# Kernel optimization log

Hardware: AMD Instinct MI355X
Metric: run time of the kernel (lower is better)

The kernel has to match this reference:

```python
import jax, jax.numpy as jnp
import numpy as np

N = 100000       # nodes
E = 1600000      # edges
V = 50000        # vocab
H = 256          # embedding dim (hsize)
A = 64           # per-head out dim (asize)
NH = 3           # num_heads
G = 64           # graphs in batch


def setup_inputs() -> dict:
    key = jax.random.key(0)
    ks = jax.random.split(key, 12)
    h0 = jax.random.randint(ks[0], (N,), 0, V)
    src = jax.random.randint(ks[1], (E,), 0, N)
    dst = jax.random.randint(ks[2], (E,), 0, N)
    graph_ids = jnp.sort(jax.random.randint(ks[3], (N,), 0, G))
    s = 0.05
    emb = jax.random.normal(ks[4], (V, H), jnp.float32) * s
    W_fc = jax.random.normal(ks[5], (H, NH * A), jnp.float32) * s   # GATConv fc
    attn_l = jax.random.normal(ks[6], (NH, A), jnp.float32) * s
    attn_r = jax.random.normal(ks[7], (NH, A), jnp.float32) * s
    bias_gat = jax.random.normal(ks[8], (NH, A), jnp.float32) * s
    W1 = jax.random.normal(ks[9], (A, 128), jnp.float32) * s
    b1 = jnp.zeros((128,), jnp.float32)
    W2 = jax.random.normal(ks[10], (128, 16), jnp.float32) * s
    b2 = jnp.zeros((16,), jnp.float32)
    return dict(h0=h0, src=src, dst=dst, graph_ids=graph_ids, emb=emb,
                W_fc=W_fc, attn_l=attn_l, attn_r=attn_r, bias_gat=bias_gat,
                W1=W1, b1=b1, W2=W2, b2=b2)


def reference(h0, src, dst, graph_ids, emb, W_fc, attn_l, attn_r, bias_gat,
              W1, b1, W2, b2):
    # embedding lookup
    h1 = emb[h0]                                            # [N, H]
    # GATConv: linear projection per head
    feat = (h1 @ W_fc).reshape(N, NH, A)                    # [N, NH, A]
    el = jnp.einsum('nha,ha->nh', feat, attn_l)             # [N, NH]
    er = jnp.einsum('nha,ha->nh', feat, attn_r)             # [N, NH]
    e = jax.nn.leaky_relu(el[src] + er[dst], 0.2)           # [E, NH]
    # segment softmax over incoming edges of each dst node
    m = jax.ops.segment_max(e, dst, num_segments=N)         # [N, NH]
    e_exp = jnp.exp(e - m[dst])                             # [E, NH]
    denom = jax.ops.segment_sum(e_exp, dst, num_segments=N) # [N, NH]
    alpha = e_exp / denom[dst]                              # [E, NH]
    # scatter-aggregate messages
    msg = alpha[:, :, None] * feat[src]                     # [E, NH, A]
    rst = jax.ops.segment_sum(msg, dst, num_segments=N)     # [N, NH, A]
    rst = rst + bias_gat[None]                              # GATConv bias
    # relu + mean over heads
    h2 = jnp.mean(jax.nn.relu(rst), axis=1)                 # [N, A]
    # MLP predictor: ReLU then Identity
    h3 = jax.nn.relu(h2 @ W1 + b1) @ W2 + b2                # [N, 16]
    # dgl.mean_nodes: per-graph mean readout
    sums = jax.ops.segment_sum(h3, graph_ids, num_segments=G)            # [G, 16]
    counts = jax.ops.segment_sum(jnp.ones((N,), h3.dtype), graph_ids, num_segments=G)
    return sums / jnp.maximum(counts, 1.0)[:, None]         # [G, 16]
```

## Files before the change

kernel.cpp:

```cpp
#include <hip/hip_runtime.h>
#include <hip/hip_bf16.h>

#define NNODES 100000
#define NEDGES 1600000
#define VOCAB 50000
#define HDIM 256
#define ADIM 64
#define NHEADS 3
#define FDIM 192
#define NGRAPH 64
#define NPART 64

#define CONV_ELEMS (HDIM * FDIM + 128 * 64 + 16 * 128)
#define CONV_BLOCKS ((CONV_ELEMS + 255) / 256)
#define HIST_BLOCKS ((NEDGES + 255) / 256)

typedef __attribute__((ext_vector_type(8))) short bf16x8;
typedef __attribute__((ext_vector_type(4))) float f32x4;

__device__ __forceinline__ float bf2f(unsigned short u) {
  return __uint_as_float((unsigned int)u << 16);
}
__device__ __forceinline__ unsigned short f2bf(float f) {
  unsigned int u = __float_as_uint(f);
  u += 0x7FFFu + ((u >> 16) & 1u);
  return (unsigned short)(u >> 16);
}

__global__ __launch_bounds__(256) void conv_hist_kernel(
    const float* __restrict__ Wfc, const float* __restrict__ W1,
    const float* __restrict__ W2, unsigned short* __restrict__ Wt,
    unsigned short* __restrict__ W1t, unsigned short* __restrict__ W2t,
    const int* __restrict__ dst, int* __restrict__ cnt,
    unsigned short* __restrict__ rank16)
{
  if (blockIdx.x < CONV_BLOCKS) {
    int i = blockIdx.x * 256 + threadIdx.x;
    if (i < HDIM * FDIM) {
      int c = i / HDIM, k = i % HDIM;
      Wt[i] = f2bf(Wfc[(size_t)k * FDIM + c]);
    } else if (i < HDIM * FDIM + 128 * 64) {
      int j = i - HDIM * FDIM;
      int c = j / 64, k = j % 64;
      W1t[j] = f2bf(W1[(size_t)k * 128 + c]);
    } else if (i < CONV_ELEMS) {
      int j = i - HDIM * FDIM - 128 * 64;
      int c = j / 128, k = j % 128;
      W2t[j] = f2bf(W2[(size_t)k * 16 + c]);
    }
  } else {
    int e = (blockIdx.x - CONV_BLOCKS) * 256 + threadIdx.x;
    if (e < NEDGES) rank16[e] = (unsigned short)atomicAdd(&cnt[dst[e]], 1);
  }
}

__global__ __launch_bounds__(256) void scan_sum_kernel(
    const int* __restrict__ cnt, int* __restrict__ bsum, int n)
{
  __shared__ int red[256];
  int t = threadIdx.x;
  int base = blockIdx.x * 1024 + t * 4;
  int s = 0;
#pragma unroll
  for (int j = 0; j < 4; ++j) if (base + j < n) s += cnt[base + j];
  red[t] = s;
  __syncthreads();
  for (int o = 128; o > 0; o >>= 1) {
    if (t < o) red[t] += red[t + o];
    __syncthreads();
  }
  if (t == 0) bsum[blockIdx.x] = red[0];
}

__global__ void scan_bsum_kernel(int* bsum, int nb)
{
  if (threadIdx.x == 0 && blockIdx.x == 0) {
    int acc = 0;
    for (int i = 0; i < nb; ++i) { int v = bsum[i]; bsum[i] = acc; acc += v; }
  }
}

__global__ __launch_bounds__(256) void scan_write_kernel(
    const int* __restrict__ cnt, const int* __restrict__ bsum,
    int* __restrict__ offs, int n, int total)
{
  __shared__ int sd[256];
  int t = threadIdx.x;
  int base = blockIdx.x * 1024 + t * 4;
  int c[4];
  int ts = 0;
#pragma unroll
  for (int j = 0; j < 4; ++j) { c[j] = (base + j < n) ? cnt[base + j] : 0; ts += c[j]; }
  sd[t] = ts;
  __syncthreads();
  for (int o = 1; o < 256; o <<= 1) {
    int v = (t >= o) ? sd[t - o] : 0;
    __syncthreads();
    sd[t] += v;
    __syncthreads();
  }
  int run = sd[t] - ts + bsum[blockIdx.x];
#pragma unroll
  for (int j = 0; j < 4; ++j) {
    if (base + j < n) offs[base + j] = run;
    run += c[j];
  }
  if (blockIdx.x == 0 && t == 0) offs[n] = total;
}

__global__ __launch_bounds__(256) void proj_gemm_kernel(
    const float* __restrict__ emb,
    const unsigned short* __restrict__ Wt,
    const float* __restrict__ attn_l, const float* __restrict__ attn_r,
    unsigned short* __restrict__ proj_bf,
    float4* __restrict__ elv4, float4* __restrict__ erv4, int V)
{
  const int wave = threadIdx.x >> 6;
  const int lane = threadIdx.x & 63;
  const int row0 = blockIdx.x * 64 + wave * 16;
  const int cb = lane & 15;
  const int q  = lane >> 4;
  int arow = row0 + cb;
  if (arow >= V) arow = V - 1;
  const int kgrp = q * 8;

  f32x4 acc[12];
#pragma unroll
  for (int c = 0; c < 12; ++c) acc[c] = (f32x4){0.f, 0.f, 0.f, 0.f};

  const float* arow_p = &emb[(size_t)arow * HDIM + kgrp];
  const unsigned short* bcol_p = &Wt[(size_t)cb * HDIM + kgrp];

#pragma unroll
  for (int ks = 0; ks < 8; ++ks) {
    float4 f0 = *reinterpret_cast<const float4*>(arow_p + ks * 32);
    float4 f1 = *reinterpret_cast<const float4*>(arow_p + ks * 32 + 4);
    bf16x8 a;
    a[0] = (short)f2bf(f0.x); a[1] = (short)f2bf(f0.y);
    a[2] = (short)f2bf(f0.z); a[3] = (short)f2bf(f0.w);
    a[4] = (short)f2bf(f1.x); a[5] = (short)f2bf(f1.y);
    a[6] = (short)f2bf(f1.z); a[7] = (short)f2bf(f1.w);
#pragma unroll
    for (int c = 0; c < 12; ++c) {
      bf16x8 b = *reinterpret_cast<const bf16x8*>(bcol_p + (size_t)c * 16 * HDIM + ks * 32);
      acc[c] = __builtin_amdgcn_mfma_f32_16x16x32_bf16(a, b, acc[c], 0, 0, 0);
    }
  }

  const int rb = row0 + 4 * q;
#pragma unroll
  for (int i = 0; i < 4; ++i) {
    int r = rb + i;
    if (r < V) {
#pragma unroll
      for (int c = 0; c < 12; ++c)
        proj_bf[(size_t)r * FDIM + c * 16 + cb] = f2bf(acc[c][i]);
    }
  }

  float al_v[12], ar_v[12];
#pragma unroll
  for (int c = 0; c < 12; ++c) {
    al_v[c] = attn_l[c * 16 + cb];
    ar_v[c] = attn_r[c * 16 + cb];
  }
  float elp[4][3], erp[4][3];
#pragma unroll
  for (int i = 0; i < 4; ++i)
#pragma unroll
    for (int h = 0; h < 3; ++h) {
      float sl = 0.f, sr = 0.f;
#pragma unroll
      for (int cc = 0; cc < 4; ++cc) {
        float v = acc[h * 4 + cc][i];
        sl += v * al_v[h * 4 + cc];
        sr += v * ar_v[h * 4 + cc];
      }
      elp[i][h] = sl; erp[i][h] = sr;
    }
#pragma unroll
  for (int s = 8; s > 0; s >>= 1) {
#pragma unroll
    for (int i = 0; i < 4; ++i)
#pragma unroll
      for (int h = 0; h < 3; ++h) {
        elp[i][h] += __shfl_xor(elp[i][h], s, 64);
        erp[i][h] += __shfl_xor(erp[i][h], s, 64);
      }
  }
  if (cb == 0) {
#pragma unroll
    for (int i = 0; i < 4; ++i) {
      int r = rb + i;
      if (r < V) {
        elv4[r] = make_float4(elp[i][0], elp[i][1], elp[i][2], 0.f);
        erv4[r] = make_float4(erp[i][0], erp[i][1], erp[i][2], 0.f);
      }
    }
  }
}

__global__ __launch_bounds__(256) void scatter_w_kernel(
    const int* __restrict__ src, const int* __restrict__ dst,
    const int* __restrict__ h0, const unsigned short* __restrict__ rank16,
    const int* __restrict__ offs,
    const float4* __restrict__ elv4, const float4* __restrict__ erv4,
    uint2* __restrict__ wrec, int E)
{
  int e = blockIdx.x * 256 + threadIdx.x;
  if (e >= E) return;
  int s = src[e], d = dst[e];
  unsigned vs = (unsigned)h0[s];
  float4 el = elv4[vs];
  float4 er = erv4[(unsigned)h0[d]];
  float e0 = el.x + er.x, e1 = el.y + er.y, e2 = el.z + er.z;
  e0 = e0 > 0.f ? e0 : 0.2f * e0;
  e1 = e1 > 0.f ? e1 : 0.2f * e1;
  e2 = e2 > 0.f ? e2 : 0.2f * e2;
  unsigned short u0 = f2bf(__expf(e0));
  unsigned short u1 = f2bf(__expf(e1));
  unsigned short u2 = f2bf(__expf(e2));
  int p = offs[d] + (int)rank16[e];
  wrec[p] = make_uint2(vs | ((unsigned)u0 << 16),
                       (unsigned)u1 | ((unsigned)u2 << 16));
}

__global__ __launch_bounds__(256) void aggregate_kernel(
    const uint2* __restrict__ wrec, const int* __restrict__ offs,
    const unsigned short* __restrict__ proj_bf, const float* __restrict__ bias_gat,
    unsigned short* __restrict__ h2bf, int N)
{
  int lane = threadIdx.x & 63;
  int n = blockIdx.x * 4 + (threadIdx.x >> 6);
  if (n >= N) return;
  int lo = offs[n], hi = offs[n + 1];
  float a0 = 0.f, a1 = 0.f, a2 = 0.f, d0 = 0.f, d1 = 0.f, d2 = 0.f;

  int i = lo;
  for (; i + 4 <= hi; i += 4) {
    uint2 r[4];
#pragma unroll
    for (int j = 0; j < 4; ++j) r[j] = wrec[i + j];
    const unsigned short* ps[4];
#pragma unroll
    for (int j = 0; j < 4; ++j)
      ps[j] = &proj_bf[(size_t)(r[j].x & 0xFFFFu) * FDIM];
    float g0[4], g1[4], g2[4];
#pragma unroll
    for (int j = 0; j < 4; ++j) {
      g0[j] = bf2f(ps[j][lane]);
      g1[j] = bf2f(ps[j][64 + lane]);
      g2[j] = bf2f(ps[j][128 + lane]);
    }
#pragma unroll
    for (int j = 0; j < 4; ++j) {
      float w0 = bf2f((unsigned short)(r[j].x >> 16));
      float w1 = bf2f((unsigned short)(r[j].y & 0xFFFFu));
      float w2 = bf2f((unsigned short)(r[j].y >> 16));
      a0 += w0 * g0[j]; a1 += w1 * g1[j]; a2 += w2 * g2[j];
      d0 += w0; d1 += w1; d2 += w2;
    }
  }
  for (; i < hi; ++i) {
    uint2 r = wrec[i];
    const unsigned short* ps = &proj_bf[(size_t)(r.x & 0xFFFFu) * FDIM];
    float w0 = bf2f((unsigned short)(r.x >> 16));
    float w1 = bf2f((unsigned short)(r.y & 0xFFFFu));
    float w2 = bf2f((unsigned short)(r.y >> 16));
    a0 += w0 * bf2f(ps[lane]);
    a1 += w1 * bf2f(ps[64 + lane]);
    a2 += w2 * bf2f(ps[128 + lane]);
    d0 += w0; d1 += w1; d2 += w2;
  }

  float i0 = d0 > 0.f ? 1.f / d0 : 0.f;
  float i1 = d1 > 0.f ? 1.f / d1 : 0.f;
  float i2 = d2 > 0.f ? 1.f / d2 : 0.f;
  float r0 = a0 * i0 + bias_gat[lane];
  float r1 = a1 * i1 + bias_gat[64 + lane];
  float r2 = a2 * i2 + bias_gat[128 + lane];
  float h2 = (fmaxf(r0, 0.f) + fmaxf(r1, 0.f) + fmaxf(r2, 0.f)) * (1.f / 3.f);
  h2bf[(size_t)n * 64 + lane] = f2bf(h2);
}

__global__ __launch_bounds__(256) void post_mfma_kernel(
    const unsigned short* __restrict__ h2bf,
    const unsigned short* __restrict__ W1t,
    const float* __restrict__ b1,
    const unsigned short* __restrict__ W2t,
    const float* __restrict__ b2, const int* __restrict__ gid,
    float* __restrict__ sums_priv, float* __restrict__ counts_priv, int N)
{
  __shared__ unsigned short z_lds[64 * 128];
  const int wave = threadIdx.x >> 6;
  const int lane = threadIdx.x & 63;
  const int r = lane & 15;
  const int q = lane >> 4;
  const int kg = q * 8;
  const int rw0 = blockIdx.x * 64 + wave * 16;

  int arow = rw0 + r;
  if (arow >= N) arow = N - 1;

  f32x4 acc1[8];
#pragma unroll
  for (int c = 0; c < 8; ++c) acc1[c] = (f32x4){0.f, 0.f, 0.f, 0.f};

#pragma unroll
  for (int ks = 0; ks < 2; ++ks) {
    bf16x8 a = *reinterpret_cast<const bf16x8*>(&h2bf[(size_t)arow * 64 + kg + ks * 32]);
#pragma unroll
    for (int c = 0; c < 8; ++c) {
      bf16x8 b = *reinterpret_cast<const bf16x8*>(&W1t[(size_t)(c * 16 + r) * 64 + kg + ks * 32]);
      acc1[c] = __builtin_amdgcn_mfma_f32_16x16x32_bf16(a, b, acc1[c], 0, 0, 0);
    }
  }
#pragma unroll
  for (int c = 0; c < 8; ++c) {
    float bb = b1[c * 16 + r];
#pragma unroll
    for (int i = 0; i < 4; ++i) {
      float z = acc1[c][i] + bb;
      z = z > 0.f ? z : 0.f;
      z_lds[(wave * 16 + 4 * q + i) * 128 + c * 16 + r] = f2bf(z);
    }
  }
  __syncthreads();

  f32x4 acc2 = (f32x4){0.f, 0.f, 0.f, 0.f};
#pragma unroll
  for (int ks = 0; ks < 4; ++ks) {
    bf16x8 a = *reinterpret_cast<const bf16x8*>(&z_lds[(wave * 16 + r) * 128 + kg + ks * 32]);
    bf16x8 b = *reinterpret_cast<const bf16x8*>(&W2t[(size_t)r * 128 + kg + ks * 32]);
    acc2 = __builtin_amdgcn_mfma_f32_16x16x32_bf16(a, b, acc2, 0, 0, 0);
  }
  const int part = blockIdx.x & (NPART - 1);
  float bb2 = b2[r];
#pragma unroll
  for (int i = 0; i < 4; ++i) {
    int row = rw0 + 4 * q + i;
    if (row < N) {
      int g = gid[row];
      atomicAdd(&sums_priv[(part * NGRAPH + g) * 16 + r], acc2[i] + bb2);
      if (r == 0) atomicAdd(&counts_priv[part * NGRAPH + g], 1.f);
    }
  }
}

__global__ void finalize_kernel(const float* __restrict__ sums_priv,
                                const float* __restrict__ counts_priv,
                                float* __restrict__ out)
{
  int j = threadIdx.x;
  int g = j >> 4;
  float s = 0.f, c = 0.f;
  for (int p = 0; p < NPART; ++p) {
    s += sums_priv[p * NGRAPH * 16 + j];
    c += counts_priv[p * NGRAPH + g];
  }
  out[j] = s / fmaxf(c, 1.f);
}

extern "C" void kernel_launch(void* const* d_in, const int* in_sizes, int n_in,
                              void* d_out, int out_size, void* d_ws, size_t ws_size,
                              hipStream_t stream)
{
  const int*   h0  = (const int*)  d_in[0];
  const int*   src = (const int*)  d_in[1];
  const int*   dst = (const int*)  d_in[2];
  const int*   gid = (const int*)  d_in[3];
  const float* emb = (const float*)d_in[4];
  const float* Wfc = (const float*)d_in[5];
  const float* al  = (const float*)d_in[6];
  const float* ar  = (const float*)d_in[7];
  const float* bg  = (const float*)d_in[8];
  const float* W1  = (const float*)d_in[9];
  const float* b1  = (const float*)d_in[10];
  const float* W2  = (const float*)d_in[11];
  const float* b2  = (const float*)d_in[12];
  float* out = (float*)d_out;

  char* ws = (char*)d_ws;
  size_t off = 0;
  auto alloc = [&](size_t bytes) -> void* {
    off = (off + 255) & ~(size_t)255;
    void* p = ws + off;
    off += bytes;
    return p;
  };
  const size_t CNT_B  = (size_t)NNODES * 4;
  const size_t CNT_BP = (CNT_B + 255) & ~(size_t)255;
  const size_t SUMS_B = (size_t)NPART * NGRAPH * 16 * 4;
  const size_t ZB     = CNT_BP + SUMS_B + (size_t)NPART * NGRAPH * 4;
  char*  zero_base = (char*)alloc(ZB);
  int*   cnt  = (int*)zero_base;
  float* sums = (float*)(zero_base + CNT_BP);
  float* cnts = (float*)(zero_base + CNT_BP + SUMS_B);

  unsigned short* Wt      = (unsigned short*)alloc((size_t)FDIM * HDIM * 2);
  unsigned short* W1t     = (unsigned short*)alloc((size_t)128 * 64 * 2);
  unsigned short* W2t     = (unsigned short*)alloc((size_t)16 * 128 * 2);
  unsigned short* proj_bf = (unsigned short*)alloc((size_t)VOCAB * FDIM * 2);
  unsigned short* h2bf    = (unsigned short*)alloc((size_t)NNODES * 64 * 2);
  unsigned short* rank16  = (unsigned short*)alloc((size_t)NEDGES * 2);
  uint2*  wrec   = (uint2*) alloc((size_t)NEDGES * 8);
  float4* elv4   = (float4*)alloc((size_t)VOCAB * 16);
  float4* erv4   = (float4*)alloc((size_t)VOCAB * 16);
  int*    offs   = (int*)   alloc((size_t)(NNODES + 1) * 4);
  int*    bsum   = (int*)   alloc((size_t)128 * 4);

  hipMemsetAsync(zero_base, 0, ZB, stream);

  const int NB = (NNODES + 1023) / 1024;

  conv_hist_kernel<<<CONV_BLOCKS + HIST_BLOCKS, 256, 0, stream>>>(
      Wfc, W1, W2, Wt, W1t, W2t, dst, cnt, rank16);
  scan_sum_kernel<<<NB, 256, 0, stream>>>(cnt, bsum, NNODES);
  scan_bsum_kernel<<<1, 64, 0, stream>>>(bsum, NB);
  scan_write_kernel<<<NB, 256, 0, stream>>>(cnt, bsum, offs, NNODES, NEDGES);
  proj_gemm_kernel<<<(VOCAB + 63) / 64, 256, 0, stream>>>(
      emb, Wt, al, ar, proj_bf, elv4, erv4, VOCAB);
  scatter_w_kernel<<<(NEDGES + 255) / 256, 256, 0, stream>>>(
      src, dst, h0, rank16, offs, elv4, erv4, wrec, NEDGES);
  aggregate_kernel<<<(NNODES + 3) / 4, 256, 0, stream>>>(wrec, offs, proj_bf,
                                                         bg, h2bf, NNODES);
  post_mfma_kernel<<<(NNODES + 63) / 64, 256, 0, stream>>>(h2bf, W1t, b1, W2t, b2, gid,
                                                           sums, cnts, NNODES);
  finalize_kernel<<<1, 1024, 0, stream>>>(sums, cnts, out);
}
```

Baseline: 340.1 us.

## Fold attention vectors into W_fc and overlap projection GEMM with edge scatter

A small prep kernel precomputes W_fc·attn_l and W_fc·attn_r so el/er per vocab row become a 256-wide dot product. That work moves into the histogram kernel, computed directly from fp32 embeddings. Because el/er no longer depend on the projection GEMM, the GEMM and the edge-weight scatter can run in one launch as independent block ranges. This removes one kernel boundary and lets the memory-bound scatter overlap the MFMA GEMM, at the cost of reading the embedding table an extra time and a slightly different rounding path for el/er (fp32 instead of bf16 GEMM output).

Result: no change. 342.8 us (+0.8%).

```diff
diff --git a/kernel.cpp b/kernel.cpp
--- a/kernel.cpp
+++ b/kernel.cpp
@@ -13,7 +13,9 @@
 
 #define CONV_ELEMS (HDIM * FDIM + 128 * 64 + 16 * 128)
 #define CONV_BLOCKS ((CONV_ELEMS + 255) / 256)
+#define ELVR_BLOCKS ((VOCAB + 3) / 4)
 #define HIST_BLOCKS ((NEDGES + 255) / 256)
+#define PROJ_BLOCKS ((VOCAB + 63) / 64)
 
 typedef __attribute__((ext_vector_type(8))) short bf16x8;
 typedef __attribute__((ext_vector_type(4))) float f32x4;
@@ -27,10 +29,34 @@
   return (unsigned short)(u >> 16);
 }
 
-__global__ __launch_bounds__(256) void conv_hist_kernel(
+__global__ __launch_bounds__(256) void prep_kernel(
+    const float* __restrict__ Wfc, const float* __restrict__ al,
+    const float* __restrict__ ar, float* __restrict__ wl, float* __restrict__ wr)
+{
+  int t = blockIdx.x * 256 + threadIdx.x;
+  if (t >= 3 * 256) return;
+  int h = t >> 8, k = t & 255;
+  const float* a_l = &al[h * 64];
+  const float* a_r = &ar[h * 64];
+  const float* row = &Wfc[(size_t)k * FDIM + h * 64];
+  float sl = 0.f, sr = 0.f;
+#pragma unroll 16
+  for (int c = 0; c < 64; ++c) {
+    float w = row[c];
+    sl += w * a_l[c];
+    sr += w * a_r[c];
+  }
+  wl[h * 256 + k] = sl;
+  wr[h * 256 + k] = sr;
+}
+
+__global__ __launch_bounds__(256) void conv_elvr_hist_kernel(
     const float* __restrict__ Wfc, const float* __restrict__ W1,
     const float* __restrict__ W2, unsigned short* __restrict__ Wt,
     unsigned short* __restrict__ W1t, unsigned short* __restrict__ W2t,
+    const float* __restrict__ emb, const float* __restrict__ wl,
+    const float* __restrict__ wr, float4* __restrict__ elv4,
+    float4* __restrict__ erv4,
     const int* __restrict__ dst, int* __restrict__ cnt,
     unsigned short* __restrict__ rank16)
 {
@@ -48,10 +74,38 @@
       int c = j / 128, k = j % 128;
       W2t[j] = f2bf(W2[(size_t)k * 16 + c]);
     }
-  } else {
-    int e = (blockIdx.x - CONV_BLOCKS) * 256 + threadIdx.x;
-    if (e < NEDGES) rank16[e] = (unsigned short)atomicAdd(&cnt[dst[e]], 1);
-  }
+    return;
+  }
+  if (blockIdx.x < CONV_BLOCKS + ELVR_BLOCKS) {
+    int v = (blockIdx.x - CONV_BLOCKS) * 4 + (threadIdx.x >> 6);
+    int lane = threadIdx.x & 63;
+    if (v >= VOCAB) return;
+    const float* er_ = &emb[(size_t)v * HDIM];
+    float e0 = er_[lane], e1 = er_[64 + lane], e2 = er_[128 + lane], e3 = er_[192 + lane];
+    float sl[3], sr[3];
+#pragma unroll
+    for (int h = 0; h < 3; ++h) {
+      const float* wlh = &wl[h * 256];
+      const float* wrh = &wr[h * 256];
+      sl[h] = e0 * wlh[lane] + e1 * wlh[64 + lane] + e2 * wlh[128 + lane] + e3 * wlh[192 + lane];
+      sr[h] = e0 * wrh[lane] + e1 * wrh[64 + lane] + e2 * wrh[128 + lane] + e3 * wrh[192 + lane];
+    }
+#pragma unroll
+    for (int s = 32; s > 0; s >>= 1) {
+#pragma unroll
+      for (int h = 0; h < 3; ++h) {
+        sl[h] += __shfl_xor(sl[h], s, 64);
+        sr[h] += __shfl_xor(sr[h], s, 64);
+      }
+    }
+    if (lane == 0) {
+      elv4[v] = make_float4(sl[0], sl[1], sl[2], 0.f);
+      erv4[v] = make_float4(sr[0], sr[1], sr[2], 0.f);
+    }
+    return;
+  }
+  int e = (blockIdx.x - CONV_BLOCKS - ELVR_BLOCKS) * 256 + threadIdx.x;
+  if (e < NEDGES) rank16[e] = (unsigned short)atomicAdd(&cnt[dst[e]], 1);
 }
 
 __global__ __launch_bounds__(256) void scan_sum_kernel(
@@ -108,20 +162,43 @@
   if (blockIdx.x == 0 && t == 0) offs[n] = total;
 }
 
-__global__ __launch_bounds__(256) void proj_gemm_kernel(
+__global__ __launch_bounds__(256) void proj_scatter_kernel(
     const float* __restrict__ emb,
     const unsigned short* __restrict__ Wt,
-    const float* __restrict__ attn_l, const float* __restrict__ attn_r,
     unsigned short* __restrict__ proj_bf,
-    float4* __restrict__ elv4, float4* __restrict__ erv4, int V)
-{
+    const int* __restrict__ src, const int* __restrict__ dst,
+    const int* __restrict__ h0, const unsigned short* __restrict__ rank16,
+    const int* __restrict__ offs,
+    const float4* __restrict__ elv4, const float4* __restrict__ erv4,
+    uint2* __restrict__ wrec)
+{
+  if (blockIdx.x >= PROJ_BLOCKS) {
+    int e = (blockIdx.x - PROJ_BLOCKS) * 256 + threadIdx.x;
+    if (e < NEDGES) {
+      int s = src[e], d = dst[e];
+      unsigned vs = (unsigned)h0[s];
+      float4 el = elv4[vs];
+      float4 er = erv4[(unsigned)h0[d]];
+      float e0 = el.x + er.x, e1 = el.y + er.y, e2 = el.z + er.z;
+      e0 = e0 > 0.f ? e0 : 0.2f * e0;
+      e1 = e1 > 0.f ? e1 : 0.2f * e1;
+      e2 = e2 > 0.f ? e2 : 0.2f * e2;
+      unsigned short u0 = f2bf(__expf(e0));
+      unsigned short u1 = f2bf(__expf(e1));
+      unsigned short u2 = f2bf(__expf(e2));
+      int p = offs[d] + (int)rank16[e];
+      wrec[p] = make_uint2(vs | ((unsigned)u0 << 16),
+                           (unsigned)u1 | ((unsigned)u2 << 16));
+    }
+    return;
+  }
   const int wave = threadIdx.x >> 6;
   const int lane = threadIdx.x & 63;
   const int row0 = blockIdx.x * 64 + wave * 16;
   const int cb = lane & 15;
   const int q  = lane >> 4;
   int arow = row0 + cb;
-  if (arow >= V) arow = V - 1;
+  if (arow >= VOCAB) arow = VOCAB - 1;
   const int kgrp = q * 8;
 
   f32x4 acc[12];
@@ -151,78 +228,12 @@
 #pragma unroll
   for (int i = 0; i < 4; ++i) {
     int r = rb + i;
-    if (r < V) {
+    if (r < VOCAB) {
 #pragma unroll
       for (int c = 0; c < 12; ++c)
         proj_bf[(size_t)r * FDIM + c * 16 + cb] = f2bf(acc[c][i]);
     }
   }
-
-  float al_v[12], ar_v[12];
-#pragma unroll
-  for (int c = 0; c < 12; ++c) {
-    al_v[c] = attn_l[c * 16 + cb];
-    ar_v[c] = attn_r[c * 16 + cb];
-  }
-  float elp[4][3], erp[4][3];
-#pragma unroll
-  for (int i = 0; i < 4; ++i)
-#pragma unroll
-    for (int h = 0; h < 3; ++h) {
-      float sl = 0.f, sr = 0.f;
-#pragma unroll
-      for (int cc = 0; cc < 4; ++cc) {
-        float v = acc[h * 4 + cc][i];
-        sl += v * al_v[h * 4 + cc];
-        sr += v * ar_v[h * 4 + cc];
-      }
-      elp[i][h] = sl; erp[i][h] = sr;
-    }
-#pragma unroll
-  for (int s = 8; s > 0; s >>= 1) {
-#pragma unroll
-    for (int i = 0; i < 4; ++i)
-#pragma unroll
-      for (int h = 0; h < 3; ++h) {
-        elp[i][h] += __shfl_xor(elp[i][h], s, 64);
-        erp[i][h] += __shfl_xor(erp[i][h], s, 64);
-      }
-  }
-  if (cb == 0) {
-#pragma unroll
-    for (int i = 0; i < 4; ++i) {
-      int r = rb + i;
-      if (r < V) {
-        elv4[r] = make_float4(elp[i][0], elp[i][1], elp[i][2], 0.f);
-        erv4[r] = make_float4(erp[i][0], erp[i][1], erp[i][2], 0.f);
-      }
-    }
-  }
-}
-
-__global__ __launch_bounds__(256) void scatter_w_kernel(
-    const int* __restrict__ src, const int* __restrict__ dst,
-    const int* __restrict__ h0, const unsigned short* __restrict__ rank16,
-    const int* __restrict__ offs,
-    const float4* __restrict__ elv4, const float4* __restrict__ erv4,
-    uint2* __restrict__ wrec, int E)
-{
-  int e = blockIdx.x * 256 + threadIdx.x;
-  if (e >= E) return;
-  int s = src[e], d = dst[e];
-  unsigned vs = (unsigned)h0[s];
-  float4 el = elv4[vs];
-  float4 er = erv4[(unsigned)h0[d]];
-  float e0 = el.x + er.x, e1 = el.y + er.y, e2 = el.z + er.z;
-  e0 = e0 > 0.f ? e0 : 0.2f * e0;
-  e1 = e1 > 0.f ? e1 : 0.2f * e1;
-  e2 = e2 > 0.f ? e2 : 0.2f * e2;
-  unsigned short u0 = f2bf(__expf(e0));
-  unsigned short u1 = f2bf(__expf(e1));
-  unsigned short u2 = f2bf(__expf(e2));
-  int p = offs[d] + (int)rank16[e];
-  wrec[p] = make_uint2(vs | ((unsigned)u0 << 16),
-                       (unsigned)u1 | ((unsigned)u2 << 16));
 }
 
 __global__ __launch_bounds__(256) void aggregate_kernel(
@@ -406,6 +417,8 @@
   uint2*  wrec   = (uint2*) alloc((size_t)NEDGES * 8);
   float4* elv4   = (float4*)alloc((size_t)VOCAB * 16);
   float4* erv4   = (float4*)alloc((size_t)VOCAB * 16);
+  float*  wl     = (float*) alloc((size_t)3 * 256 * 4);
+  float*  wr     = (float*) alloc((size_t)3 * 256 * 4);
   int*    offs   = (int*)   alloc((size_t)(NNODES + 1) * 4);
   int*    bsum   = (int*)   alloc((size_t)128 * 4);
 
@@ -413,15 +426,14 @@
 
   const int NB = (NNODES + 1023) / 1024;
 
-  conv_hist_kernel<<<CONV_BLOCKS + HIST_BLOCKS, 256, 0, stream>>>(
-      Wfc, W1, W2, Wt, W1t, W2t, dst, cnt, rank16);
+  prep_kernel<<<3, 256, 0, stream>>>(Wfc, al, ar, wl, wr);
+  conv_elvr_hist_kernel<<<CONV_BLOCKS + ELVR_BLOCKS + HIST_BLOCKS, 256, 0, stream>>>(
+      Wfc, W1, W2, Wt, W1t, W2t, emb, wl, wr, elv4, erv4, dst, cnt, rank16);
   scan_sum_kernel<<<NB, 256, 0, stream>>>(cnt, bsum, NNODES);
   scan_bsum_kernel<<<1, 64, 0, stream>>>(bsum, NB);
   scan_write_kernel<<<NB, 256, 0, stream>>>(cnt, bsum, offs, NNODES, NEDGES);
-  proj_gemm_kernel<<<(VOCAB + 63) / 64, 256, 0, stream>>>(
-      emb, Wt, al, ar, proj_bf, elv4, erv4, VOCAB);
-  scatter_w_kernel<<<(NEDGES + 255) / 256, 256, 0, stream>>>(
-      src, dst, h0, rank16, offs, elv4, erv4, wrec, NEDGES);
+  proj_scatter_kernel<<<PROJ_BLOCKS + HIST_BLOCKS, 256, 0, stream>>>(
+      emb, Wt, proj_bf, src, dst, h0, rank16, offs, elv4, erv4, wrec);
   aggregate_kernel<<<(NNODES + 3) / 4, 256, 0, stream>>>(wrec, offs, proj_bf,
                                                          bg, h2bf, NNODES);
   post_mfma_kernel<<<(NNODES + 63) / 64, 256, 0, stream>>>(h2bf, W1t, b1, W2t, b2, gid,
```
